# Kernel tuning notes

Measured on AMD Instinct MI355X. Metric: run time of the kernel, lower is better.

The kernel has to match this reference:

```python
import jax, jax.numpy as jnp
import numpy as np

B = 16384   # batch (agents x parallel envs)
IN = 12     # input_dim
H = 64      # hidden_dim -> 2H = 128
OUT = 25    # output_dim (forced by x[:,0:5]..x[:,20:25] slicing)


def setup_inputs() -> dict:
    key = jax.random.key(0)
    ks = jax.random.split(key, 24)
    n = lambda k, s: jax.random.normal(k, s, dtype=jnp.float32)
    s = 0.1  # scale params to keep SiLU/softmax in a sane range
    return {
        "x": n(ks[0], (B, IN)),
        "na": 4,
        # mlp_in: Linear(IN, 2H) + SiLU
        "W_in": n(ks[1], (2 * H, IN)) * s, "b_in": n(ks[2], (2 * H,)) * s,
        # first attention (2H)
        "Aq4": n(ks[3], (2 * H, 2 * H)) * s, "Bq4": n(ks[4], (2 * H,)) * s,
        "Ak4": n(ks[5], (2 * H, 2 * H)) * s, "Bk4": n(ks[6], (2 * H,)) * s,
        "Av4": n(ks[7], (2 * H, 2 * H)) * s, "Bv4": n(ks[8], (2 * H,)) * s,
        # mlp_hidden_4: Linear(2H, H) + SiLU
        "W_h": n(ks[9], (H, 2 * H)) * s, "b_h": n(ks[10], (H,)) * s,
        # second attention (H)
        "Aq7": n(ks[11], (H, H)) * s, "Bq7": n(ks[12], (H,)) * s,
        "Ak7": n(ks[13], (H, H)) * s, "Bk7": n(ks[14], (H,)) * s,
        "Av7": n(ks[15], (H, H)) * s, "Bv7": n(ks[16], (H,)) * s,
        # mlp_out: Linear(H, OUT) + SiLU
        "W_out": n(ks[17], (OUT, H)) * s, "b_out": n(ks[18], (OUT,)) * s,
    }


def _attn(h, Aq, Bq, Ak, Bk, Av, Bv):
    # h: [B, D]; torch does bmm(A, x^T)+B with x of shape [B,1,D] -> seq-len-1
    # attention, i.e. scores are an outer product q k^T of shape [B, D, D].
    q = jax.nn.silu(h @ Aq.T + Bq)                      # [B, D]
    k = jax.nn.silu(h @ Ak.T + Bk)                      # [B, D]
    v = jax.nn.silu(h @ Av.T + Bv)                      # [B, D]
    a = jax.nn.softmax(q[:, :, None] * k[:, None, :], axis=2)  # [B, D, D]
    return jax.nn.silu(jnp.einsum("bij,bj->bi", a, v))  # [B, D]


def reference(x, na, W_in, b_in, Aq4, Bq4, Ak4, Bk4, Av4, Bv4,
              W_h, b_h, Aq7, Bq7, Ak7, Bk7, Av7, Bv7, W_out, b_out):
    h = jax.nn.silu(x @ W_in.T + b_in)                  # [B, 2H]
    h = _attn(h, Aq4, Bq4, Ak4, Bk4, Av4, Bv4)          # [B, 2H]
    h = jax.nn.silu(h @ W_h.T + b_h)                    # [B, H]
    h = _attn(h, Aq7, Bq7, Ak7, Bk7, Av7, Bv7)          # [B, H]
    y = jax.nn.silu(h @ W_out.T + b_out)                # [B, 25]

    # block-diagonal quadratic-form assembly (l=2, kron with ones(1,2))
    M11 = jnp.sum(y[:, 0:5] ** 2, axis=1)               # [B]
    M12 = jnp.sum(y[:, 5:10] ** 2, axis=1)
    M21 = jnp.sum(y[:, 10:15] ** 2, axis=1)
    M22 = jnp.sum(y[:, 15:20] ** 2, axis=1)
    Mpp = jnp.sum(y[:, 20:25] ** 2, axis=1)             # [B]
    q = y[:, :4]                                        # [B, 4] = [q0,q1,q2,q3]
    # M = [[diag(M11), diag(M12)],[diag(M21), diag(M22)]] (each 2x2 diag)
    quad = (M11 * (q[:, 0] ** 2 + q[:, 1] ** 2)
            + (M12 + M21) * (q[:, 0] * q[:, 2] + q[:, 1] * q[:, 3])
            + M22 * (q[:, 2] ** 2 + q[:, 3] ** 2))
    return (quad + Mpp)[:, None]                        # [B, 1]
```

## Files before the change

kernel.cpp:

```cpp
#include <hip/hip_runtime.h>

#define RPW 4
#define WAVES 4
#define RPB (RPW * WAVES)
#define NM 14

using short8 = __attribute__((ext_vector_type(8))) short;
using f32x4  = __attribute__((ext_vector_type(4))) float;

#define LOG2E 1.4426950408889634f

static __device__ __forceinline__ float ex2(float x) { return __builtin_amdgcn_exp2f(x); }
static __device__ __forceinline__ float rcpf_(float x) { return __builtin_amdgcn_rcpf(x); }
static __device__ __forceinline__ float silu_(float x) {
    return x * rcpf_(1.0f + ex2(-x * LOG2E));
}
static __device__ __forceinline__ unsigned short bfhi(float x) {
    return (unsigned short)(__float_as_uint(x) >> 16);
}
static __device__ __forceinline__ unsigned short bfrn(float x) {
    unsigned u = __float_as_uint(x);
    return (unsigned short)((u + 0x7fffu + ((u >> 16) & 1u)) >> 16);
}
static __device__ __forceinline__ float bf2f(unsigned short h) {
    return __uint_as_float(((unsigned)h) << 16);
}

__constant__ float c_invfact[15] = {
    1.f, 1.f, 0.5f, 1.f/6, 1.f/24, 1.f/120, 1.f/720, 1.f/5040, 1.f/40320,
    1.f/362880, 1.f/3628800, 1.f/39916800, 1.f/479001600,
    1.f/6227020800.f, 1.f/87178291200.f};

template <int O, int I>
__device__ __forceinline__ void tr(const float* __restrict__ s, float* __restrict__ d,
                                   int t0, int stride) {
    for (int idx = t0; idx < O * I; idx += stride) {
        int o = idx / I, in = idx - o * I;
        d[in * O + o] = s[idx];
    }
}
template <int N>
__device__ __forceinline__ void cvt(const float* __restrict__ s,
                                    unsigned short* __restrict__ hi,
                                    unsigned short* __restrict__ lo,
                                    int t0, int stride) {
    for (int i = t0; i < N; i += stride) {
        float a = s[i];
        unsigned short h = bfhi(a);
        float r = a - bf2f(h);
        hi[i] = h;
        lo[i] = bfhi(r);
    }
}

__global__ void tweights(const float* __restrict__ s0, const float* __restrict__ s1,
                         const float* __restrict__ s2, const float* __restrict__ s3,
                         const float* __restrict__ s4, const float* __restrict__ s5,
                         const float* __restrict__ s6, const float* __restrict__ s7,
                         const float* __restrict__ s8, float* __restrict__ ws) {
    const int stride = gridDim.x * blockDim.x;
    const int t0 = blockIdx.x * blockDim.x + threadIdx.x;
    tr<128, 12>(s0, ws + 0, t0, stride);
    unsigned short* u4 = (unsigned short*)(ws + 1536);
    cvt<128 * 128>(s1, u4 + 0,     u4 + 16384, t0, stride);
    cvt<128 * 128>(s2, u4 + 32768, u4 + 49152, t0, stride);
    cvt<128 * 128>(s3, u4 + 65536, u4 + 81920, t0, stride);
    unsigned short* wh = (unsigned short*)(ws + 50688);
    cvt<64 * 128>(s4, wh + 0, wh + 8192, t0, stride);
    unsigned short* u7 = (unsigned short*)(ws + 58880);
    cvt<64 * 64>(s5, u7 + 0,     u7 + 4096,  t0, stride);
    cvt<64 * 64>(s6, u7 + 8192,  u7 + 12288, t0, stride);
    cvt<64 * 64>(s7, u7 + 16384, u7 + 20480, t0, stride);
    tr<25, 64>(s8, ws + 71168, t0, stride);
}

__global__ __launch_bounds__(256, 4) void fused_net(
    const float* __restrict__ x, const float* __restrict__ ws,
    const float* __restrict__ b_in,
    const float* __restrict__ Bq4, const float* __restrict__ Bk4, const float* __restrict__ Bv4,
    const float* __restrict__ b_h,
    const float* __restrict__ Bq7, const float* __restrict__ Bk7, const float* __restrict__ Bv7,
    const float* __restrict__ b_out,
    float* __restrict__ out) {
    __shared__ __align__(16) unsigned short hAhi[16][136], hAlo[16][136];
    __shared__ __align__(16) unsigned short h2hi[16][80],  h2lo[16][80];
    __shared__ __align__(16) float sQ[16][132];
    __shared__ __align__(16) unsigned short sKVb[16][132][2];
    __shared__ __align__(16) float h3T[WAVES][64][RPW];
    __shared__ __align__(16) float sXT[WAVES][12][RPW];
    __shared__ __align__(16) float sY[WAVES][RPW][26];

    const int tid = threadIdx.x;
    const int w = tid >> 6;
    const int l = tid & 63;
    const int row0 = blockIdx.x * RPB + w * RPW;
    const int m16 = l & 15, quad = l >> 4;
    const int g = l & 15, r = l >> 4;
    const int R = w * RPW + r;

    const float* WinT  = ws + 0;
    const float* WoutT = ws + 71168;

    if (l < 12 * RPW) {
        float v = x[row0 * 12 + l];
        int rr = l / 12, in = l - rr * 12;
        sXT[w][in][rr] = v;
    }

    {
        float2 bb = *(const float2*)&b_in[2 * l];
        float a0[RPW], a1[RPW];
        #pragma unroll
        for (int rr = 0; rr < RPW; rr++) { a0[rr] = bb.x; a1[rr] = bb.y; }
        #pragma unroll
        for (int in = 0; in < 12; in++) {
            float2 wv = *(const float2*)&WinT[in * 128 + 2 * l];
            float4 xr = *(const float4*)&sXT[w][in][0];
            a0[0] = fmaf(xr.x, wv.x, a0[0]); a1[0] = fmaf(xr.x, wv.y, a1[0]);
            a0[1] = fmaf(xr.y, wv.x, a0[1]); a1[1] = fmaf(xr.y, wv.y, a1[1]);
            a0[2] = fmaf(xr.z, wv.x, a0[2]); a1[2] = fmaf(xr.z, wv.y, a1[2]);
            a0[3] = fmaf(xr.w, wv.x, a0[3]); a1[3] = fmaf(xr.w, wv.y, a1[3]);
        }
        #pragma unroll
        for (int rr = 0; rr < RPW; rr++) {
            float h0 = silu_(a0[rr]), h1 = silu_(a1[rr]);
            unsigned short h0h = bfhi(h0), h1h = bfhi(h1);
            float r0 = h0 - bf2f(h0h), r1 = h1 - bf2f(h1h);
            *(unsigned*)&hAhi[w * 4 + rr][2 * l] = (unsigned)h0h | ((unsigned)h1h << 16);
            *(unsigned*)&hAlo[w * 4 + rr][2 * l] = (unsigned)bfhi(r0) | ((unsigned)bfhi(r1) << 16);
        }
    }
    __syncthreads();

    {
        short8 Ah[4], Al[4];
        #pragma unroll
        for (int kt = 0; kt < 4; kt++) {
            Ah[kt] = *(const short8*)&hAhi[m16][kt * 32 + quad * 8];
            Al[kt] = *(const short8*)&hAlo[m16][kt * 32 + quad * 8];
        }
        const unsigned short* u4 = (const unsigned short*)(ws + 1536);
        #pragma unroll
        for (int t = 0; t < 6; t++) {
            const int nt = w * 6 + t;
            const int mat = nt >> 3;
            const int n = (nt & 7) * 16 + m16;
            const float* bp = (mat == 0) ? Bq4 : (mat == 1) ? Bk4 : Bv4;
            float b = bp[n];
            f32x4 acc = {b, b, b, b};
            const unsigned short* Bh = u4 + mat * 32768 + n * 128;
            const unsigned short* Bl = Bh + 16384;
            #pragma unroll
            for (int kt = 0; kt < 4; kt++) {
                short8 bh = *(const short8*)&Bh[kt * 32 + quad * 8];
                short8 bl = *(const short8*)&Bl[kt * 32 + quad * 8];
                acc = __builtin_amdgcn_mfma_f32_16x16x32_bf16(Ah[kt], bh, acc, 0, 0, 0);
                acc = __builtin_amdgcn_mfma_f32_16x16x32_bf16(Ah[kt], bl, acc, 0, 0, 0);
                acc = __builtin_amdgcn_mfma_f32_16x16x32_bf16(Al[kt], bh, acc, 0, 0, 0);
            }
            #pragma unroll
            for (int reg = 0; reg < 4; reg++) {
                int row = quad * 4 + reg;
                float val = silu_(acc[reg]);
                if (mat == 0)      sQ[row][n] = val;
                else if (mat == 1) sKVb[row][n][0] = bfrn(val);
                else               sKVb[row][n][1] = bfrn(val);
            }
        }
    }
    __syncthreads();

    {
        float dmom[NM];
        float nmom[NM + 1];
        #pragma unroll
        for (int m = 0; m < NM; m++) dmom[m] = 0.f;
        #pragma unroll
        for (int m = 0; m <= NM; m++) nmom[m] = 0.f;
        uint4 u0 = *(const uint4*)&sKVb[R][g * 8][0];
        uint4 u1 = *(const uint4*)&sKVb[R][g * 8 + 4][0];
        unsigned us[8] = {u0.x, u0.y, u0.z, u0.w, u1.x, u1.y, u1.z, u1.w};
        #pragma unroll
        for (int jj = 0; jj < 8; jj++) {
            unsigned u = us[jj];
            float kf = __uint_as_float(u << 16);
            float vf = __uint_as_float(u & 0xffff0000u);
            nmom[0] += vf;
            float p = kf;
            dmom[0] += p; nmom[1] = fmaf(vf, p, nmom[1]);
            #pragma unroll
            for (int m = 1; m < NM; m++) {
                p *= kf;
                dmom[m] += p;
                nmom[m + 1] = fmaf(vf, p, nmom[m + 1]);
            }
        }
        #pragma unroll
        for (int m = 0; m < NM; m++) {
            float v = dmom[m];
            v += __shfl_xor(v, 1); v += __shfl_xor(v, 2);
            v += __shfl_xor(v, 4); v += __shfl_xor(v, 8);
            dmom[m] = v;
        }
        #pragma unroll
        for (int m = 0; m <= NM; m++) {
            float v = nmom[m];
            v += __shfl_xor(v, 1); v += __shfl_xor(v, 2);
            v += __shfl_xor(v, 4); v += __shfl_xor(v, 8);
            nmom[m] = v;
        }
        float cd[NM + 1], cn[NM + 1];
        cd[0] = 128.f; cn[0] = nmom[0];
        #pragma unroll
        for (int m = 1; m <= NM; m++) {
            cd[m] = dmom[m - 1] * c_invfact[m];
            cn[m] = nmom[m] * c_invfact[m];
        }
        float4 qa = *(const float4*)&sQ[R][g * 8];
        float4 qb = *(const float4*)&sQ[R][g * 8 + 4];
        float qs[8] = {qa.x, qa.y, qa.z, qa.w, qb.x, qb.y, qb.z, qb.w};
        unsigned hiw[4], low[4];
        #pragma unroll
        for (int i = 0; i < 8; i++) {
            float t = qs[i];
            float d = cd[NM], nn = cn[NM];
            #pragma unroll
            for (int m = NM - 1; m >= 0; m--) {
                d = fmaf(d, t, cd[m]);
                nn = fmaf(nn, t, cn[m]);
            }
            float o = silu_(nn * rcpf_(d));
            unsigned short oh = bfhi(o);
            unsigned short olo = bfhi(o - bf2f(oh));
            if (i & 1) { hiw[i >> 1] |= ((unsigned)oh) << 16; low[i >> 1] |= ((unsigned)olo) << 16; }
            else       { hiw[i >> 1] = oh; low[i >> 1] = olo; }
        }
        *(uint4*)&hAhi[R][g * 8] = make_uint4(hiw[0], hiw[1], hiw[2], hiw[3]);
        *(uint4*)&hAlo[R][g * 8] = make_uint4(low[0], low[1], low[2], low[3]);
    }
    __syncthreads();

    {
        short8 Ah[4], Al[4];
        #pragma unroll
        for (int kt = 0; kt < 4; kt++) {
            Ah[kt] = *(const short8*)&hAhi[m16][kt * 32 + quad * 8];
            Al[kt] = *(const short8*)&hAlo[m16][kt * 32 + quad * 8];
        }
        const unsigned short* whh = (const unsigned short*)(ws + 50688);
        const unsigned short* whl = whh + 8192;
        const int n = w * 16 + m16;
        float b = b_h[n];
        f32x4 acc = {b, b, b, b};
        #pragma unroll
        for (int kt = 0; kt < 4; kt++) {
            short8 bh = *(const short8*)&whh[n * 128 + kt * 32 + quad * 8];
            short8 bl = *(const short8*)&whl[n * 128 + kt * 32 + quad * 8];
            acc = __builtin_amdgcn_mfma_f32_16x16x32_bf16(Ah[kt], bh, acc, 0, 0, 0);
            acc = __builtin_amdgcn_mfma_f32_16x16x32_bf16(Ah[kt], bl, acc, 0, 0, 0);
            acc = __builtin_amdgcn_mfma_f32_16x16x32_bf16(Al[kt], bh, acc, 0, 0, 0);
        }
        #pragma unroll
        for (int reg = 0; reg < 4; reg++) {
            int row = quad * 4 + reg;
            float hv = silu_(acc[reg]);
            unsigned short hh = bfhi(hv);
            h2hi[row][n] = hh;
            h2lo[row][n] = bfhi(hv - bf2f(hh));
        }
    }
    __syncthreads();

    {
        short8 Ah[2], Al[2];
        #pragma unroll
        for (int kt = 0; kt < 2; kt++) {
            Ah[kt] = *(const short8*)&h2hi[m16][kt * 32 + quad * 8];
            Al[kt] = *(const short8*)&h2lo[m16][kt * 32 + quad * 8];
        }
        const unsigned short* u7 = (const unsigned short*)(ws + 58880);
        #pragma unroll
        for (int t = 0; t < 3; t++) {
            const int nt = w * 3 + t;
            const int mat = nt >> 2;
            const int n = (nt & 3) * 16 + m16;
            const float* bp = (mat == 0) ? Bq7 : (mat == 1) ? Bk7 : Bv7;
            float b = bp[n];
            f32x4 acc = {b, b, b, b};
            const unsigned short* Bh = u7 + mat * 8192 + n * 64;
            const unsigned short* Bl = Bh + 4096;
            #pragma unroll
            for (int kt = 0; kt < 2; kt++) {
                short8 bh = *(const short8*)&Bh[kt * 32 + quad * 8];
                short8 bl = *(const short8*)&Bl[kt * 32 + quad * 8];
                acc = __builtin_amdgcn_mfma_f32_16x16x32_bf16(Ah[kt], bh, acc, 0, 0, 0);
                acc = __builtin_amdgcn_mfma_f32_16x16x32_bf16(Ah[kt], bl, acc, 0, 0, 0);
                acc = __builtin_amdgcn_mfma_f32_16x16x32_bf16(Al[kt], bh, acc, 0, 0, 0);
            }
            #pragma unroll
            for (int reg = 0; reg < 4; reg++) {
                int row = quad * 4 + reg;
                float val = silu_(acc[reg]);
                if (mat == 0)      sQ[row][n] = val;
                else if (mat == 1) sKVb[row][n][0] = bfrn(val);
                else               sKVb[row][n][1] = bfrn(val);
            }
        }
    }
    __syncthreads();

    {
        float dmom[NM];
        float nmom[NM + 1];
        #pragma unroll
        for (int m = 0; m < NM; m++) dmom[m] = 0.f;
        #pragma unroll
        for (int m = 0; m <= NM; m++) nmom[m] = 0.f;
        uint4 u0 = *(const uint4*)&sKVb[R][g * 4][0];
        unsigned us[4] = {u0.x, u0.y, u0.z, u0.w};
        #pragma unroll
        for (int jj = 0; jj < 4; jj++) {
            unsigned u = us[jj];
            float kf = __uint_as_float(u << 16);
            float vf = __uint_as_float(u & 0xffff0000u);
            nmom[0] += vf;
            float p = kf;
            dmom[0] += p; nmom[1] = fmaf(vf, p, nmom[1]);
            #pragma unroll
            for (int m = 1; m < NM; m++) {
                p *= kf;
                dmom[m] += p;
                nmom[m + 1] = fmaf(vf, p, nmom[m + 1]);
            }
        }
        #pragma unroll
        for (int m = 0; m < NM; m++) {
            float v = dmom[m];
            v += __shfl_xor(v, 1); v += __shfl_xor(v, 2);
            v += __shfl_xor(v, 4); v += __shfl_xor(v, 8);
            dmom[m] = v;
        }
        #pragma unroll
        for (int m = 0; m <= NM; m++) {
            float v = nmom[m];
            v += __shfl_xor(v, 1); v += __shfl_xor(v, 2);
            v += __shfl_xor(v, 4); v += __shfl_xor(v, 8);
            nmom[m] = v;
        }
        float cd[NM + 1], cn[NM + 1];
        cd[0] = 64.f; cn[0] = nmom[0];
        #pragma unroll
        for (int m = 1; m <= NM; m++) {
            cd[m] = dmom[m - 1] * c_invfact[m];
            cn[m] = nmom[m] * c_invfact[m];
        }
        float4 qa = *(const float4*)&sQ[R][g * 4];
        float qs[4] = {qa.x, qa.y, qa.z, qa.w};
        #pragma unroll
        for (int i = 0; i < 4; i++) {
            float t = qs[i];
            float d = cd[NM], nn = cn[NM];
            #pragma unroll
            for (int m = NM - 1; m >= 0; m--) {
                d = fmaf(d, t, cd[m]);
                nn = fmaf(nn, t, cn[m]);
            }
            h3T[w][g * 4 + i][r] = silu_(nn * rcpf_(d));
        }
    }

    {
        const int o = l & 31;
        const int half = l >> 5;
        const int oc = (o < 25) ? o : 0;
        float y[RPW];
        float bb = (half == 0) ? b_out[oc] : 0.f;
        #pragma unroll
        for (int rr = 0; rr < RPW; rr++) y[rr] = bb;
        const int in0 = half * 32;
        #pragma unroll 4
        for (int i = 0; i < 32; i++) {
            int in = in0 + i;
            float wv = WoutT[in * 25 + oc];
            float4 xr = *(const float4*)&h3T[w][in][0];
            y[0] = fmaf(xr.x, wv, y[0]);
            y[1] = fmaf(xr.y, wv, y[1]);
            y[2] = fmaf(xr.z, wv, y[2]);
            y[3] = fmaf(xr.w, wv, y[3]);
        }
        #pragma unroll
        for (int rr = 0; rr < RPW; rr++) {
            float full = y[rr] + __shfl_xor(y[rr], 32, 64);
            if (l < 25) sY[w][rr][l] = silu_(full);
        }
    }

    if (l < RPW) {
        const int rr = l;
        float y[25];
        #pragma unroll
        for (int c = 0; c < 25; c++) y[c] = sY[w][rr][c];
        float M11 = 0.f, M12 = 0.f, M21 = 0.f, M22 = 0.f, Mpp = 0.f;
        #pragma unroll
        for (int c = 0; c < 5; c++) {
            M11 = fmaf(y[c], y[c], M11);
            M12 = fmaf(y[5 + c], y[5 + c], M12);
            M21 = fmaf(y[10 + c], y[10 + c], M21);
            M22 = fmaf(y[15 + c], y[15 + c], M22);
            Mpp = fmaf(y[20 + c], y[20 + c], Mpp);
        }
        float quad = M11 * (y[0] * y[0] + y[1] * y[1])
                   + (M12 + M21) * (y[0] * y[2] + y[1] * y[3])
                   + M22 * (y[2] * y[2] + y[3] * y[3]);
        out[row0 + rr] = quad + Mpp;
    }
}

extern "C" void kernel_launch(void* const* d_in, const int* in_sizes, int n_in,
                              void* d_out, int out_size, void* d_ws, size_t ws_size,
                              hipStream_t stream) {
    const float* x    = (const float*)d_in[0];
    const float* W_in = (const float*)d_in[2];
    const float* b_in = (const float*)d_in[3];
    const float* Aq4  = (const float*)d_in[4];
    const float* Bq4  = (const float*)d_in[5];
    const float* Ak4  = (const float*)d_in[6];
    const float* Bk4  = (const float*)d_in[7];
    const float* Av4  = (const float*)d_in[8];
    const float* Bv4  = (const float*)d_in[9];
    const float* W_h  = (const float*)d_in[10];
    const float* b_h  = (const float*)d_in[11];
    const float* Aq7  = (const float*)d_in[12];
    const float* Bq7  = (const float*)d_in[13];
    const float* Ak7  = (const float*)d_in[14];
    const float* Bk7  = (const float*)d_in[15];
    const float* Av7  = (const float*)d_in[16];
    const float* Bv7  = (const float*)d_in[17];
    const float* Wout = (const float*)d_in[18];
    const float* bout = (const float*)d_in[19];
    float* ws = (float*)d_ws;

    tweights<<<128, 256, 0, stream>>>(W_in, Aq4, Ak4, Av4, W_h, Aq7, Ak7, Av7, Wout, ws);

    const int B = in_sizes[0] / 12;
    const int grid = B / RPB;
    fused_net<<<grid, 256, 0, stream>>>(x, ws, b_in, Bq4, Bk4, Bv4,
                                        b_h, Bq7, Bk7, Bv7, bout, (float*)d_out);
}
```

Baseline: 137.9 us.

## Make each wave independent with per-wave scratch and drop block barriers

Each wave now owns its own shared-memory scratch and computes every output tile of each MFMA GEMM for its 4 rows, instead of splitting the N tiles across the 4 waves of a 16-row block. This removes all __syncthreads between stages. The cost is redundant MFMA work: each 16x16 tile now carries only 4 useful rows (m16&3 duplicates them), so each wave issues 4x more MFMAs and weight loads. Only quad 0 writes the results.

```diff
diff --git a/kernel.cpp b/kernel.cpp
--- a/kernel.cpp
+++ b/kernel.cpp
@@ -1,7 +1,7 @@
 #include <hip/hip_runtime.h>
 
+#define WAVES 4
 #define RPW 4
-#define WAVES 4
 #define RPB (RPW * WAVES)
 #define NM 14
 
@@ -74,6 +74,18 @@
     tr<25, 64>(s8, ws + 71168, t0, stride);
 }
 
+struct WaveScratch {
+    unsigned short hAhi[4][136];
+    unsigned short hAlo[4][136];
+    unsigned short h2hi[4][80];
+    unsigned short h2lo[4][80];
+    float sQ[4][132];
+    unsigned short sKV[4][132][2];
+    float h3T[64][4];
+    float sXT[12][4];
+    float sY[4][26];
+};
+
 __global__ __launch_bounds__(256, 4) void fused_net(
     const float* __restrict__ x, const float* __restrict__ ws,
     const float* __restrict__ b_in,
@@ -82,13 +94,7 @@
     const float* __restrict__ Bq7, const float* __restrict__ Bk7, const float* __restrict__ Bv7,
     const float* __restrict__ b_out,
     float* __restrict__ out) {
-    __shared__ __align__(16) unsigned short hAhi[16][136], hAlo[16][136];
-    __shared__ __align__(16) unsigned short h2hi[16][80],  h2lo[16][80];
-    __shared__ __align__(16) float sQ[16][132];
-    __shared__ __align__(16) unsigned short sKVb[16][132][2];
-    __shared__ __align__(16) float h3T[WAVES][64][RPW];
-    __shared__ __align__(16) float sXT[WAVES][12][RPW];
-    __shared__ __align__(16) float sY[WAVES][RPW][26];
+    __shared__ __align__(16) WaveScratch S[WAVES];
 
     const int tid = threadIdx.x;
     const int w = tid >> 6;
@@ -96,15 +102,15 @@
     const int row0 = blockIdx.x * RPB + w * RPW;
     const int m16 = l & 15, quad = l >> 4;
     const int g = l & 15, r = l >> 4;
-    const int R = w * RPW + r;
-
+
+    WaveScratch& Sw = S[w];
     const float* WinT  = ws + 0;
     const float* WoutT = ws + 71168;
 
     if (l < 12 * RPW) {
         float v = x[row0 * 12 + l];
         int rr = l / 12, in = l - rr * 12;
-        sXT[w][in][rr] = v;
+        Sw.sXT[in][rr] = v;
     }
 
     {
@@ -115,7 +121,7 @@
         #pragma unroll
         for (int in = 0; in < 12; in++) {
             float2 wv = *(const float2*)&WinT[in * 128 + 2 * l];
-            float4 xr = *(const float4*)&sXT[w][in][0];
+            float4 xr = *(const float4*)&Sw.sXT[in][0];
             a0[0] = fmaf(xr.x, wv.x, a0[0]); a1[0] = fmaf(xr.x, wv.y, a1[0]);
             a0[1] = fmaf(xr.y, wv.x, a0[1]); a1[1] = fmaf(xr.y, wv.y, a1[1]);
             a0[2] = fmaf(xr.z, wv.x, a0[2]); a1[2] = fmaf(xr.z, wv.y, a1[2]);
@@ -126,25 +132,23 @@
             float h0 = silu_(a0[rr]), h1 = silu_(a1[rr]);
             unsigned short h0h = bfhi(h0), h1h = bfhi(h1);
             float r0 = h0 - bf2f(h0h), r1 = h1 - bf2f(h1h);
-            *(unsigned*)&hAhi[w * 4 + rr][2 * l] = (unsigned)h0h | ((unsigned)h1h << 16);
-            *(unsigned*)&hAlo[w * 4 + rr][2 * l] = (unsigned)bfhi(r0) | ((unsigned)bfhi(r1) << 16);
-        }
-    }
-    __syncthreads();
+            *(unsigned*)&Sw.hAhi[rr][2 * l] = (unsigned)h0h | ((unsigned)h1h << 16);
+            *(unsigned*)&Sw.hAlo[rr][2 * l] = (unsigned)bfhi(r0) | ((unsigned)bfhi(r1) << 16);
+        }
+    }
 
     {
         short8 Ah[4], Al[4];
         #pragma unroll
         for (int kt = 0; kt < 4; kt++) {
-            Ah[kt] = *(const short8*)&hAhi[m16][kt * 32 + quad * 8];
-            Al[kt] = *(const short8*)&hAlo[m16][kt * 32 + quad * 8];
+            Ah[kt] = *(const short8*)&Sw.hAhi[m16 & 3][kt * 32 + quad * 8];
+            Al[kt] = *(const short8*)&Sw.hAlo[m16 & 3][kt * 32 + quad * 8];
         }
         const unsigned short* u4 = (const unsigned short*)(ws + 1536);
-        #pragma unroll
-        for (int t = 0; t < 6; t++) {
-            const int nt = w * 6 + t;
-            const int mat = nt >> 3;
-            const int n = (nt & 7) * 16 + m16;
+        #pragma unroll 4
+        for (int t = 0; t < 24; t++) {
+            const int mat = t >> 3;
+            const int n = (t & 7) * 16 + m16;
             const float* bp = (mat == 0) ? Bq4 : (mat == 1) ? Bk4 : Bv4;
             float b = bp[n];
             f32x4 acc = {b, b, b, b};
@@ -158,17 +162,17 @@
                 acc = __builtin_amdgcn_mfma_f32_16x16x32_bf16(Ah[kt], bl, acc, 0, 0, 0);
                 acc = __builtin_amdgcn_mfma_f32_16x16x32_bf16(Al[kt], bh, acc, 0, 0, 0);
             }
-            #pragma unroll
-            for (int reg = 0; reg < 4; reg++) {
-                int row = quad * 4 + reg;
-                float val = silu_(acc[reg]);
-                if (mat == 0)      sQ[row][n] = val;
-                else if (mat == 1) sKVb[row][n][0] = bfrn(val);
-                else               sKVb[row][n][1] = bfrn(val);
-            }
-        }
-    }
-    __syncthreads();
+            if (quad == 0) {
+                #pragma unroll
+                for (int reg = 0; reg < 4; reg++) {
+                    float val = silu_(acc[reg]);
+                    if (mat == 0)      Sw.sQ[reg][n] = val;
+                    else if (mat == 1) Sw.sKV[reg][n][0] = bfrn(val);
+                    else               Sw.sKV[reg][n][1] = bfrn(val);
+                }
+            }
+        }
+    }
 
     {
         float dmom[NM];
@@ -177,8 +181,8 @@
         for (int m = 0; m < NM; m++) dmom[m] = 0.f;
         #pragma unroll
         for (int m = 0; m <= NM; m++) nmom[m] = 0.f;
-        uint4 u0 = *(const uint4*)&sKVb[R][g * 8][0];
-        uint4 u1 = *(const uint4*)&sKVb[R][g * 8 + 4][0];
+        uint4 u0 = *(const uint4*)&Sw.sKV[r][g * 8][0];
+        uint4 u1 = *(const uint4*)&Sw.sKV[r][g * 8 + 4][0];
         unsigned us[8] = {u0.x, u0.y, u0.z, u0.w, u1.x, u1.y, u1.z, u1.w};
         #pragma unroll
         for (int jj = 0; jj < 8; jj++) {
@@ -216,8 +220,8 @@
             cd[m] = dmom[m - 1] * c_invfact[m];
             cn[m] = nmom[m] * c_invfact[m];
         }
-        float4 qa = *(const float4*)&sQ[R][g * 8];
-        float4 qb = *(const float4*)&sQ[R][g * 8 + 4];
+        float4 qa = *(const float4*)&Sw.sQ[r][g * 8];
+        float4 qb = *(const float4*)&Sw.sQ[r][g * 8 + 4];
         float qs[8] = {qa.x, qa.y, qa.z, qa.w, qb.x, qb.y, qb.z, qb.w};
         unsigned hiw[4], low[4];
         #pragma unroll
@@ -235,55 +239,56 @@
             if (i & 1) { hiw[i >> 1] |= ((unsigned)oh) << 16; low[i >> 1] |= ((unsigned)olo) << 16; }
             else       { hiw[i >> 1] = oh; low[i >> 1] = olo; }
         }
-        *(uint4*)&hAhi[R][g * 8] = make_uint4(hiw[0], hiw[1], hiw[2], hiw[3]);
-        *(uint4*)&hAlo[R][g * 8] = make_uint4(low[0], low[1], low[2], low[3]);
-    }
-    __syncthreads();
+        *(uint4*)&Sw.hAhi[r][g * 8] = make_uint4(hiw[0], hiw[1], hiw[2], hiw[3]);
+        *(uint4*)&Sw.hAlo[r][g * 8] = make_uint4(low[0], low[1], low[2], low[3]);
+    }
 
     {
         short8 Ah[4], Al[4];
         #pragma unroll
         for (int kt = 0; kt < 4; kt++) {
-            Ah[kt] = *(const short8*)&hAhi[m16][kt * 32 + quad * 8];
-            Al[kt] = *(const short8*)&hAlo[m16][kt * 32 + quad * 8];
+            Ah[kt] = *(const short8*)&Sw.hAhi[m16 & 3][kt * 32 + quad * 8];
+            Al[kt] = *(const short8*)&Sw.hAlo[m16 & 3][kt * 32 + quad * 8];
         }
         const unsigned short* whh = (const unsigned short*)(ws + 50688);
         const unsigned short* whl = whh + 8192;
-        const int n = w * 16 + m16;
-        float b = b_h[n];
-        f32x4 acc = {b, b, b, b};
-        #pragma unroll
-        for (int kt = 0; kt < 4; kt++) {
-            short8 bh = *(const short8*)&whh[n * 128 + kt * 32 + quad * 8];
-            short8 bl = *(const short8*)&whl[n * 128 + kt * 32 + quad * 8];
-            acc = __builtin_amdgcn_mfma_f32_16x16x32_bf16(Ah[kt], bh, acc, 0, 0, 0);
-            acc = __builtin_amdgcn_mfma_f32_16x16x32_bf16(Ah[kt], bl, acc, 0, 0, 0);
-            acc = __builtin_amdgcn_mfma_f32_16x16x32_bf16(Al[kt], bh, acc, 0, 0, 0);
-        }
-        #pragma unroll
-        for (int reg = 0; reg < 4; reg++) {
-            int row = quad * 4 + reg;
-            float hv = silu_(acc[reg]);
-            unsigned short hh = bfhi(hv);
-            h2hi[row][n] = hh;
-            h2lo[row][n] = bfhi(hv - bf2f(hh));
-        }
-    }
-    __syncthreads();
+        #pragma unroll
+        for (int t = 0; t < 4; t++) {
+            const int n = t * 16 + m16;
+            float b = b_h[n];
+            f32x4 acc = {b, b, b, b};
+            #pragma unroll
+            for (int kt = 0; kt < 4; kt++) {
+                short8 bh = *(const short8*)&whh[n * 128 + kt * 32 + quad * 8];
+                short8 bl = *(const short8*)&whl[n * 128 + kt * 32 + quad * 8];
+                acc = __builtin_amdgcn_mfma_f32_16x16x32_bf16(Ah[kt], bh, acc, 0, 0, 0);
+                acc = __builtin_amdgcn_mfma_f32_16x16x32_bf16(Ah[kt], bl, acc, 0, 0, 0);
+                acc = __builtin_amdgcn_mfma_f32_16x16x32_bf16(Al[kt], bh, acc, 0, 0, 0);
+            }
+            if (quad == 0) {
+                #pragma unroll
+                for (int reg = 0; reg < 4; reg++) {
+                    float hv = silu_(acc[reg]);
+                    unsigned short hh = bfhi(hv);
+                    Sw.h2hi[reg][n] = hh;
+                    Sw.h2lo[reg][n] = bfhi(hv - bf2f(hh));
+                }
+            }
+        }
+    }
 
     {
         short8 Ah[2], Al[2];
         #pragma unroll
         for (int kt = 0; kt < 2; kt++) {
-            Ah[kt] = *(const short8*)&h2hi[m16][kt * 32 + quad * 8];
-            Al[kt] = *(const short8*)&h2lo[m16][kt * 32 + quad * 8];
+            Ah[kt] = *(const short8*)&Sw.h2hi[m16 & 3][kt * 32 + quad * 8];
+            Al[kt] = *(const short8*)&Sw.h2lo[m16 & 3][kt * 32 + quad * 8];
         }
         const unsigned short* u7 = (const unsigned short*)(ws + 58880);
-        #pragma unroll
-        for (int t = 0; t < 3; t++) {
-            const int nt = w * 3 + t;
-            const int mat = nt >> 2;
-            const int n = (nt & 3) * 16 + m16;
+        #pragma unroll 4
+        for (int t = 0; t < 12; t++) {
+            const int mat = t >> 2;
+            const int n = (t & 3) * 16 + m16;
             const float* bp = (mat == 0) ? Bq7 : (mat == 1) ? Bk7 : Bv7;
             float b = bp[n];
             f32x4 acc = {b, b, b, b};
@@ -297,17 +302,17 @@
                 acc = __builtin_amdgcn_mfma_f32_16x16x32_bf16(Ah[kt], bl, acc, 0, 0, 0);
                 acc = __builtin_amdgcn_mfma_f32_16x16x32_bf16(Al[kt], bh, acc, 0, 0, 0);
             }
-            #pragma unroll
-            for (int reg = 0; reg < 4; reg++) {
-                int row = quad * 4 + reg;
-                float val = silu_(acc[reg]);
-                if (mat == 0)      sQ[row][n] = val;
-                else if (mat == 1) sKVb[row][n][0] = bfrn(val);
-                else               sKVb[row][n][1] = bfrn(val);
-            }
-        }
-    }
-    __syncthreads();
+            if (quad == 0) {
+                #pragma unroll
+                for (int reg = 0; reg < 4; reg++) {
+                    float val = silu_(acc[reg]);
+                    if (mat == 0)      Sw.sQ[reg][n] = val;
+                    else if (mat == 1) Sw.sKV[reg][n][0] = bfrn(val);
+                    else               Sw.sKV[reg][n][1] = bfrn(val);
+                }
+            }
+        }
+    }
 
     {
         float dmom[NM];
@@ -316,7 +321,7 @@
         for (int m = 0; m < NM; m++) dmom[m] = 0.f;
         #pragma unroll
         for (int m = 0; m <= NM; m++) nmom[m] = 0.f;
-        uint4 u0 = *(const uint4*)&sKVb[R][g * 4][0];
+        uint4 u0 = *(const uint4*)&Sw.sKV[r][g * 4][0];
         unsigned us[4] = {u0.x, u0.y, u0.z, u0.w};
         #pragma unroll
         for (int jj = 0; jj < 4; jj++) {
@@ -354,7 +359,7 @@
             cd[m] = dmom[m - 1] * c_invfact[m];
             cn[m] = nmom[m] * c_invfact[m];
         }
-        float4 qa = *(const float4*)&sQ[R][g * 4];
+        float4 qa = *(const float4*)&Sw.sQ[r][g * 4];
         float qs[4] = {qa.x, qa.y, qa.z, qa.w};
         #pragma unroll
         for (int i = 0; i < 4; i++) {
@@ -365,7 +370,7 @@
                 d = fmaf(d, t, cd[m]);
                 nn = fmaf(nn, t, cn[m]);
             }
-            h3T[w][g * 4 + i][r] = silu_(nn * rcpf_(d));
+            Sw.h3T[g * 4 + i][r] = silu_(nn * rcpf_(d));
         }
     }
 
@@ -382,7 +387,7 @@
         for (int i = 0; i < 32; i++) {
             int in = in0 + i;
             float wv = WoutT[in * 25 + oc];
-            float4 xr = *(const float4*)&h3T[w][in][0];
+            float4 xr = *(const float4*)&Sw.h3T[in][0];
             y[0] = fmaf(xr.x, wv, y[0]);
             y[1] = fmaf(xr.y, wv, y[1]);
             y[2] = fmaf(xr.z, wv, y[2]);
@@ -391,7 +396,7 @@
         #pragma unroll
         for (int rr = 0; rr < RPW; rr++) {
             float full = y[rr] + __shfl_xor(y[rr], 32, 64);
-            if (l < 25) sY[w][rr][l] = silu_(full);
+            if (l < 25) Sw.sY[rr][l] = silu_(full);
         }
     }
 
@@ -399,7 +404,7 @@
         const int rr = l;
         float y[25];
         #pragma unroll
-        for (int c = 0; c < 25; c++) y[c] = sY[w][rr][c];
+        for (int c = 0; c < 25; c++) y[c] = Sw.sY[rr][c];
         float M11 = 0.f, M12 = 0.f, M21 = 0.f, M22 = 0.f, Mpp = 0.f;
         #pragma unroll
         for (int c = 0; c < 5; c++) {
```

Measured after the change: 224.1 us. +62.5%, slower.
